# Optimization experiments

Hardware: AMD Instinct MI355X
Metric: run time of the kernel (lower is better)

The kernel has to match this reference:

```python
import jax, jax.numpy as jnp
import numpy as np

DET = 512       # detector bins
N_THETA = 180   # projection angles, theta = 0..179 degrees (1 deg spacing)


def _ramp_filter(size):
    """skimage _get_fourier_filter(size, 'ramp'): spatial ramp -> FFT."""
    n = np.concatenate((np.arange(1, size // 2 + 1, 2),
                        np.arange(size // 2 - 1, 0, -2)))
    f = np.zeros(size)
    f[0] = 0.25
    f[1::2] = -1.0 / (np.pi * n) ** 2
    return jnp.asarray(2.0 * np.real(np.fft.fft(f)), dtype=jnp.float32)


def _iradon(x):
    B, C, det, A = x.shape
    theta = jnp.deg2rad(jnp.arange(A, dtype=jnp.float32))  # 0..179 deg

    # --- ramp filtering along the detector axis ---
    size = max(64, int(2 ** np.ceil(np.log2(2 * det))))  # 1024 for det=512
    filt = _ramp_filter(size)                            # (size,)
    xp = jnp.pad(x, ((0, 0), (0, 0), (0, size - det), (0, 0)))
    proj_f = jnp.fft.fft(xp, axis=2) * filt[None, None, :, None]
    filtered = jnp.real(jnp.fft.ifft(proj_f, axis=2))[:, :, :det, :]  # (B,C,det,A)

    # --- backprojection (circle=False) ---
    out_size = int(np.floor(np.sqrt(det ** 2 / 2.0)))  # 362
    radius = out_size // 2
    xpr = jnp.arange(out_size, dtype=jnp.float32)[:, None] - radius  # rows
    ypr = jnp.arange(out_size, dtype=jnp.float32)[None, :] - radius  # cols
    cos_t = jnp.cos(theta)
    sin_t = jnp.sin(theta)
    # detector coordinate for every (angle, pixel): t = y*cos - x*sin
    t = ypr[None] * cos_t[:, None, None] - xpr[None] * sin_t[:, None, None]  # (A,out,out)
    pos = t + det // 2          # index into detector axis (x = arange(det)-det//2)
    i0 = jnp.floor(pos).astype(jnp.int32)
    frac = pos - i0.astype(jnp.float32)
    in_range = ((pos >= 0) & (pos <= det - 1)).astype(jnp.float32)  # fill_value=0 outside
    i0c = jnp.clip(i0, 0, det - 1)
    i1c = jnp.clip(i0 + 1, 0, det - 1)

    P = out_size * out_size
    ft = jnp.moveaxis(filtered, 3, 2)                     # (B,C,A,det)
    idx0 = jnp.broadcast_to(i0c.reshape(A, P)[None, None], (B, C, A, P))
    idx1 = jnp.broadcast_to(i1c.reshape(A, P)[None, None], (B, C, A, P))
    g0 = jnp.take_along_axis(ft, idx0, axis=3)            # (B,C,A,P)
    g1 = jnp.take_along_axis(ft, idx1, axis=3)
    w = frac.reshape(A, P)[None, None]
    m = in_range.reshape(A, P)[None, None]
    val = ((1.0 - w) * g0 + w * g1) * m                   # bilinear-in-1D interp, 0 outside
    recon = val.sum(axis=2).reshape(B, C, out_size, out_size)
    return recon * (jnp.pi / (2.0 * A))


def setup_inputs() -> dict:
    key = jax.random.key(0)
    x = jax.random.normal(key, (4, 1, DET, N_THETA), dtype=jnp.float32)
    return {"x": x}


def reference(x):
    return _iradon(x)
```

## Files before the change

### kernel.cpp

```cpp
#include <hip/hip_runtime.h>
#include <math.h>

#define DET 512
#define NA  180
#define OUT 362
#define RAD 181
#define OUTSQ (OUT * OUT)
#define NB  4

#define NSPLIT 12
#define APB    15
#define CHUNK  5
#define LQ     514

constexpr double PI_D = 3.14159265358979323846;

constexpr double tsin(double x) {
    double x2 = x * x;
    return x * (1.0 + x2 * (-1.0/6 + x2 * (1.0/120 + x2 * (-1.0/5040 +
               x2 * (1.0/362880 + x2 * (-1.0/39916800))))));
}
constexpr double tcos(double x) {
    double x2 = x * x;
    return 1.0 + x2 * (-0.5 + x2 * (1.0/24 + x2 * (-1.0/720 +
               x2 * (1.0/40320 + x2 * (-1.0/3628800)))));
}

struct Trig { float c[NA]; float s[NA]; };
constexpr Trig make_trig() {
    Trig t{};
    constexpr double r = PI_D / 180.0;
    for (int k = 0; k < NA; ++k) {
        double c, s;
        if (k <= 45)       { c =  tcos(k * r);          s =  tsin(k * r); }
        else if (k <= 90)  { c =  tsin((90 - k) * r);   s =  tcos((90 - k) * r); }
        else if (k <= 135) { c = -tsin((k - 90) * r);   s =  tcos((k - 90) * r); }
        else               { c = -tcos((180 - k) * r);  s =  tsin((180 - k) * r); }
        t.c[k] = (float)c; t.s[k] = (float)s;
    }
    return t;
}
__device__ constexpr Trig TRIG = make_trig();

__host__ __device__ constexpr float rampw0(int m) {
    int a = m < 0 ? -m : m;
    if (a > 511 || (a & 1) == 0) return 0.0f;
    double md = (double)a;
    return (float)(-2.0 / (PI_D * PI_D * md * md));
}

template<int R>
__device__ __forceinline__ void tap(const float* __restrict__ p,
        float& a0, float& a1, float& a2, float& a3) {
    const float v = p[R];
    if constexpr (rampw0(R)      != 0.0f) a0 = fmaf(rampw0(R),      v, a0);
    if constexpr (rampw0(R - 32) != 0.0f) a1 = fmaf(rampw0(R - 32), v, a1);
    if constexpr (rampw0(R - 64) != 0.0f) a2 = fmaf(rampw0(R - 64), v, a2);
    if constexpr (rampw0(R - 96) != 0.0f) a3 = fmaf(rampw0(R - 96), v, a3);
}

template<int R, int REND>
__device__ __forceinline__ void sweep(const float* __restrict__ p,
        float& a0, float& a1, float& a2, float& a3) {
    if constexpr (R <= REND) {
        tap<R>(p, a0, a1, a2, a3);
        sweep<R + 2, REND>(p, a0, a1, a2, a3);
    }
}

__global__ __launch_bounds__(512) void ramp_filter_kernel(
        const float* __restrict__ x, float* __restrict__ ft) {
    const int a   = blockIdx.x;
    const int b   = blockIdx.y;
    const int tid = threadIdx.x;
    const int t   = tid & 127;
    const int qtr = tid >> 7;
    const int q = (t & 31) + 128 * (t >> 5);

    __shared__ float xs[3 * DET];
    __shared__ float red[3][4][128];

    xs[tid]        = 0.0f;
    xs[1024 + tid] = 0.0f;
    xs[512 + tid]  = x[(b * DET + tid) * NA + a];
    __syncthreads();

    const float* p = xs + 512 + q;
    float a0 = 0.0f, a1 = 0.0f, a2 = 0.0f, a3 = 0.0f;

    if (qtr == 0) {
        a0 = 0.5f * p[0];
        a1 = 0.5f * p[32];
        a2 = 0.5f * p[64];
        a3 = 0.5f * p[96];
        sweep<-511, -233>(p, a0, a1, a2, a3);
    } else if (qtr == 1) {
        sweep<-231, 47>(p, a0, a1, a2, a3);
    } else if (qtr == 2) {
        sweep<49, 327>(p, a0, a1, a2, a3);
    } else {
        sweep<329, 607>(p, a0, a1, a2, a3);
    }
    if (qtr != 0) {
        red[qtr - 1][0][t] = a0;
        red[qtr - 1][1][t] = a1;
        red[qtr - 1][2][t] = a2;
        red[qtr - 1][3][t] = a3;
    }
    __syncthreads();

    if (qtr == 0) {
        float* ob = ft + ((size_t)a * DET + q) * NB + b;
        ob[0 * 4 * NB / 4 * 0] = 0.0f;
        ob[0]        = a0 + red[0][0][t] + red[1][0][t] + red[2][0][t];
        ob[32 * NB]  = a1 + red[0][1][t] + red[1][1][t] + red[2][1][t];
        ob[64 * NB]  = a2 + red[0][2][t] + red[1][2][t] + red[2][2][t];
        ob[96 * NB]  = a3 + red[0][3][t] + red[1][3][t] + red[2][3][t];
    }
}

__device__ __forceinline__ void acc4(float4& acc,
        const float4* __restrict__ L, float pos) {
    float pf = floorf(pos);
    float fr = pos - pf;
    int   i0 = (int)pf;
    const float4* q = (pos > (float)(DET - 1)) ? (L + DET) : (L + i0);
    float4 g0 = q[0];
    float4 g1 = q[1];
    acc.x += fmaf(fr, g1.x - g0.x, g0.x);
    acc.y += fmaf(fr, g1.y - g0.y, g0.y);
    acc.z += fmaf(fr, g1.z - g0.z, g0.z);
    acc.w += fmaf(fr, g1.w - g0.w, g0.w);
}

__global__ __launch_bounds__(256) void backproject_kernel(
        const float4* __restrict__ ftq, float* __restrict__ out) {
    const int sp = blockIdx.z;
    const int r0 = blockIdx.y * 32;
    const int c0 = blockIdx.x * 32;
    const int tid = threadIdx.x;
    const int tx = tid & 15;
    const int ty = tid >> 4;

    __shared__ float4 lines[CHUNK][LQ];

    if (tid < 2 * CHUNK)
        lines[tid >> 1][DET + (tid & 1)] = float4{0.0f, 0.0f, 0.0f, 0.0f};

    const float xpr = (float)(min(r0 + ty, OUT - 1) - RAD);
    const float ypr = (float)(min(c0 + tx, OUT - 1) - RAD);

    float4 a00 = {0,0,0,0}, a01 = {0,0,0,0}, a10 = {0,0,0,0}, a11 = {0,0,0,0};

    for (int rd = 0; rd < APB / CHUNK; ++rd) {
        __syncthreads();
        const float4* g = ftq + (size_t)(sp * APB + rd * CHUNK) * DET;
        #pragma unroll
        for (int k = 0; k < CHUNK * DET / 256; ++k) {
            int j = tid + k * 256;
            lines[j >> 9][j & 511] = g[j];
        }
        __syncthreads();

        const int abase = sp * APB + rd * CHUNK;
        #pragma unroll
        for (int i = 0; i < CHUNK; ++i) {
            const float cv = TRIG.c[abase + i];
            const float sv = TRIG.s[abase + i];
            float p00 = fmaf(ypr, cv, fmaf(xpr, -sv, 256.0f));
            float p01 = fmaf(16.0f, cv, p00);
            float p10 = fmaf(-16.0f, sv, p00);
            float p11 = fmaf(-16.0f, sv, p01);
            const float4* L = &lines[i][0];
            acc4(a00, L, p00);
            acc4(a01, L, p01);
            acc4(a10, L, p10);
            acc4(a11, L, p11);
        }
    }

    const float scale = (float)(PI_D / (2.0 * NA));
    const int r = r0 + ty;
    const int c = c0 + tx;

#define EMIT(ACC, RR, CC)                                          \
    if ((RR) < OUT && (CC) < OUT) {                                \
        const int off = (RR) * OUT + (CC);                         \
        atomicAdd(out + off,             (ACC).x * scale);         \
        atomicAdd(out + OUTSQ + off,     (ACC).y * scale);         \
        atomicAdd(out + 2 * OUTSQ + off, (ACC).z * scale);         \
        atomicAdd(out + 3 * OUTSQ + off, (ACC).w * scale);         \
    }
    EMIT(a00, r, c);
    EMIT(a01, r, c + 16);
    EMIT(a10, r + 16, c);
    EMIT(a11, r + 16, c + 16);
#undef EMIT
}

extern "C" void kernel_launch(void* const* d_in, const int* in_sizes, int n_in,
                              void* d_out, int out_size, void* d_ws, size_t ws_size,
                              hipStream_t stream) {
    const float* x = (const float*)d_in[0];
    float* ft  = (float*)d_ws;
    float* out = (float*)d_out;

    const int B = in_sizes[0] / (DET * NA);

    hipMemsetAsync(out, 0, (size_t)out_size * sizeof(float), stream);
    ramp_filter_kernel<<<dim3(NA, B), 512, 0, stream>>>(x, ft);
    backproject_kernel<<<dim3((OUT + 31) / 32, (OUT + 31) / 32, NSPLIT),
                         256, 0, stream>>>((const float4*)ft, out);
}
```

Measured before the change: 107.6 us.

## Restructure ramp filter to 8 outputs per thread and widen backprojection tiles

The ramp filter now splits the convolution across 8 tap ranges, with each thread computing 8 outputs spaced 64 bins apart, and reduces the partial sums through a larger shared array. This is meant to balance work per thread and cut redundant shared loads. Backprojection moves to 512-thread blocks covering 32x64 pixel tiles, with each thread handling 4 pixels in a row and a smaller angle chunk in shared memory. Fewer blocks reload the filtered lines, at the cost of higher register pressure, less parallelism in the reduction thread, and more wasted threads at the column edge.

```diff
diff --git a/kernel.cpp b/kernel.cpp
--- a/kernel.cpp
+++ b/kernel.cpp
@@ -10,7 +10,7 @@
 
 #define NSPLIT 12
 #define APB    15
-#define CHUNK  5
+#define CHUNK  3
 #define LQ     514
 
 constexpr double PI_D = 3.14159265358979323846;
@@ -50,21 +50,23 @@
 }
 
 template<int R>
-__device__ __forceinline__ void tap(const float* __restrict__ p,
-        float& a0, float& a1, float& a2, float& a3) {
+__device__ __forceinline__ void tap8(const float* __restrict__ p, float* acc) {
     const float v = p[R];
-    if constexpr (rampw0(R)      != 0.0f) a0 = fmaf(rampw0(R),      v, a0);
-    if constexpr (rampw0(R - 32) != 0.0f) a1 = fmaf(rampw0(R - 32), v, a1);
-    if constexpr (rampw0(R - 64) != 0.0f) a2 = fmaf(rampw0(R - 64), v, a2);
-    if constexpr (rampw0(R - 96) != 0.0f) a3 = fmaf(rampw0(R - 96), v, a3);
+    if constexpr (rampw0(R)       != 0.0f) acc[0] = fmaf(rampw0(R),       v, acc[0]);
+    if constexpr (rampw0(R - 64)  != 0.0f) acc[1] = fmaf(rampw0(R - 64),  v, acc[1]);
+    if constexpr (rampw0(R - 128) != 0.0f) acc[2] = fmaf(rampw0(R - 128), v, acc[2]);
+    if constexpr (rampw0(R - 192) != 0.0f) acc[3] = fmaf(rampw0(R - 192), v, acc[3]);
+    if constexpr (rampw0(R - 256) != 0.0f) acc[4] = fmaf(rampw0(R - 256), v, acc[4]);
+    if constexpr (rampw0(R - 320) != 0.0f) acc[5] = fmaf(rampw0(R - 320), v, acc[5]);
+    if constexpr (rampw0(R - 384) != 0.0f) acc[6] = fmaf(rampw0(R - 384), v, acc[6]);
+    if constexpr (rampw0(R - 448) != 0.0f) acc[7] = fmaf(rampw0(R - 448), v, acc[7]);
 }
 
 template<int R, int REND>
-__device__ __forceinline__ void sweep(const float* __restrict__ p,
-        float& a0, float& a1, float& a2, float& a3) {
+__device__ __forceinline__ void sweep8(const float* __restrict__ p, float* acc) {
     if constexpr (R <= REND) {
-        tap<R>(p, a0, a1, a2, a3);
-        sweep<R + 2, REND>(p, a0, a1, a2, a3);
+        tap8<R>(p, acc);
+        sweep8<R + 2, REND>(p, acc);
     }
 }
 
@@ -73,49 +75,47 @@
     const int a   = blockIdx.x;
     const int b   = blockIdx.y;
     const int tid = threadIdx.x;
-    const int t   = tid & 127;
-    const int qtr = tid >> 7;
-    const int q = (t & 31) + 128 * (t >> 5);
+    const int t   = tid & 63;
+    const int e   = tid >> 6;
 
     __shared__ float xs[3 * DET];
-    __shared__ float red[3][4][128];
+    __shared__ float red[7][8][64];
 
     xs[tid]        = 0.0f;
     xs[1024 + tid] = 0.0f;
     xs[512 + tid]  = x[(b * DET + tid) * NA + a];
     __syncthreads();
 
-    const float* p = xs + 512 + q;
-    float a0 = 0.0f, a1 = 0.0f, a2 = 0.0f, a3 = 0.0f;
-
-    if (qtr == 0) {
-        a0 = 0.5f * p[0];
-        a1 = 0.5f * p[32];
-        a2 = 0.5f * p[64];
-        a3 = 0.5f * p[96];
-        sweep<-511, -233>(p, a0, a1, a2, a3);
-    } else if (qtr == 1) {
-        sweep<-231, 47>(p, a0, a1, a2, a3);
-    } else if (qtr == 2) {
-        sweep<49, 327>(p, a0, a1, a2, a3);
-    } else {
-        sweep<329, 607>(p, a0, a1, a2, a3);
-    }
-    if (qtr != 0) {
-        red[qtr - 1][0][t] = a0;
-        red[qtr - 1][1][t] = a1;
-        red[qtr - 1][2][t] = a2;
-        red[qtr - 1][3][t] = a3;
+    const float* p = xs + 512 + t;
+    float acc[8] = {0.0f, 0.0f, 0.0f, 0.0f, 0.0f, 0.0f, 0.0f, 0.0f};
+
+    if (e == 0) {
+        #pragma unroll
+        for (int j = 0; j < 8; ++j) acc[j] = 0.5f * p[64 * j];
+        sweep8<-511, -329>(p, acc);
+    } else if (e == 1) { sweep8<-327, -145>(p, acc);
+    } else if (e == 2) { sweep8<-143,   39>(p, acc);
+    } else if (e == 3) { sweep8<  41,  223>(p, acc);
+    } else if (e == 4) { sweep8< 225,  407>(p, acc);
+    } else if (e == 5) { sweep8< 409,  591>(p, acc);
+    } else if (e == 6) { sweep8< 593,  775>(p, acc);
+    } else             { sweep8< 777,  959>(p, acc); }
+
+    if (e != 0) {
+        #pragma unroll
+        for (int j = 0; j < 8; ++j) red[e - 1][j][t] = acc[j];
     }
     __syncthreads();
 
-    if (qtr == 0) {
-        float* ob = ft + ((size_t)a * DET + q) * NB + b;
-        ob[0 * 4 * NB / 4 * 0] = 0.0f;
-        ob[0]        = a0 + red[0][0][t] + red[1][0][t] + red[2][0][t];
-        ob[32 * NB]  = a1 + red[0][1][t] + red[1][1][t] + red[2][1][t];
-        ob[64 * NB]  = a2 + red[0][2][t] + red[1][2][t] + red[2][2][t];
-        ob[96 * NB]  = a3 + red[0][3][t] + red[1][3][t] + red[2][3][t];
+    if (e == 0) {
+        float* ob = ft + ((size_t)a * DET + t) * NB + b;
+        #pragma unroll
+        for (int j = 0; j < 8; ++j) {
+            float s = acc[j];
+            #pragma unroll
+            for (int q7 = 0; q7 < 7; ++q7) s += red[q7][j][t];
+            ob[(size_t)(64 * j) * NB] = s;
+        }
     }
 }
 
@@ -133,11 +133,11 @@
     acc.w += fmaf(fr, g1.w - g0.w, g0.w);
 }
 
-__global__ __launch_bounds__(256) void backproject_kernel(
+__global__ __launch_bounds__(512, 6) void backproject_kernel(
         const float4* __restrict__ ftq, float* __restrict__ out) {
     const int sp = blockIdx.z;
     const int r0 = blockIdx.y * 32;
-    const int c0 = blockIdx.x * 32;
+    const int c0 = blockIdx.x * 64;
     const int tid = threadIdx.x;
     const int tx = tid & 15;
     const int ty = tid >> 4;
@@ -148,16 +148,16 @@
         lines[tid >> 1][DET + (tid & 1)] = float4{0.0f, 0.0f, 0.0f, 0.0f};
 
     const float xpr = (float)(min(r0 + ty, OUT - 1) - RAD);
-    const float ypr = (float)(min(c0 + tx, OUT - 1) - RAD);
-
-    float4 a00 = {0,0,0,0}, a01 = {0,0,0,0}, a10 = {0,0,0,0}, a11 = {0,0,0,0};
+    const float ypr = (float)(c0 + tx - RAD);
+
+    float4 A0 = {0,0,0,0}, A1 = {0,0,0,0}, A2 = {0,0,0,0}, A3 = {0,0,0,0};
 
     for (int rd = 0; rd < APB / CHUNK; ++rd) {
         __syncthreads();
         const float4* g = ftq + (size_t)(sp * APB + rd * CHUNK) * DET;
         #pragma unroll
-        for (int k = 0; k < CHUNK * DET / 256; ++k) {
-            int j = tid + k * 256;
+        for (int k = 0; k < CHUNK; ++k) {
+            int j = tid + k * 512;
             lines[j >> 9][j & 511] = g[j];
         }
         __syncthreads();
@@ -167,34 +167,33 @@
         for (int i = 0; i < CHUNK; ++i) {
             const float cv = TRIG.c[abase + i];
             const float sv = TRIG.s[abase + i];
-            float p00 = fmaf(ypr, cv, fmaf(xpr, -sv, 256.0f));
-            float p01 = fmaf(16.0f, cv, p00);
-            float p10 = fmaf(-16.0f, sv, p00);
-            float p11 = fmaf(-16.0f, sv, p01);
+            float p0 = fmaf(ypr, cv, fmaf(xpr, -sv, 256.0f));
+            float p1 = fmaf(16.0f, cv, p0);
+            float p2 = fmaf(32.0f, cv, p0);
+            float p3 = fmaf(48.0f, cv, p0);
             const float4* L = &lines[i][0];
-            acc4(a00, L, p00);
-            acc4(a01, L, p01);
-            acc4(a10, L, p10);
-            acc4(a11, L, p11);
+            acc4(A0, L, p0);
+            acc4(A1, L, p1);
+            acc4(A2, L, p2);
+            acc4(A3, L, p3);
         }
     }
 
     const float scale = (float)(PI_D / (2.0 * NA));
     const int r = r0 + ty;
-    const int c = c0 + tx;
-
-#define EMIT(ACC, RR, CC)                                          \
-    if ((RR) < OUT && (CC) < OUT) {                                \
-        const int off = (RR) * OUT + (CC);                         \
+
+#define EMIT(ACC, CC)                                              \
+    if (r < OUT && (CC) < OUT) {                                   \
+        const int off = r * OUT + (CC);                            \
         atomicAdd(out + off,             (ACC).x * scale);         \
         atomicAdd(out + OUTSQ + off,     (ACC).y * scale);         \
         atomicAdd(out + 2 * OUTSQ + off, (ACC).z * scale);         \
         atomicAdd(out + 3 * OUTSQ + off, (ACC).w * scale);         \
     }
-    EMIT(a00, r, c);
-    EMIT(a01, r, c + 16);
-    EMIT(a10, r + 16, c);
-    EMIT(a11, r + 16, c + 16);
+    EMIT(A0, c0 + tx);
+    EMIT(A1, c0 + tx + 16);
+    EMIT(A2, c0 + tx + 32);
+    EMIT(A3, c0 + tx + 48);
 #undef EMIT
 }
 
@@ -209,6 +208,6 @@
 
     hipMemsetAsync(out, 0, (size_t)out_size * sizeof(float), stream);
     ramp_filter_kernel<<<dim3(NA, B), 512, 0, stream>>>(x, ft);
-    backproject_kernel<<<dim3((OUT + 31) / 32, (OUT + 31) / 32, NSPLIT),
-                         256, 0, stream>>>((const float4*)ft, out);
-}
+    backproject_kernel<<<dim3((OUT + 63) / 64, (OUT + 31) / 32, NSPLIT),
+                         512, 0, stream>>>((const float4*)ft, out);
+}
```

New measurement: 118.6 us. 1.1x slower.

## Pad shared-memory line stride to 5 floats and halve ramp filter block

Applied to the files above, without the earlier changes.

The backprojection kernel now stores each detector bin's four batch values at a stride of five floats in shared memory instead of as packed float4s. This is meant to reduce LDS bank conflicts on the data-dependent gathers, at the cost of scalar loads instead of 128-bit loads. To fit the padded layout, the chunk of staged angles per round drops from five to three. The ramp filter kernel moves from 512 to 256 threads, with each thread doing twice as many taps and a smaller two-way reduction.

```diff
diff --git a/kernel.cpp b/kernel.cpp
--- a/kernel.cpp
+++ b/kernel.cpp
@@ -10,8 +10,9 @@
 
 #define NSPLIT 12
 #define APB    15
-#define CHUNK  5
-#define LQ     514
+#define CHUNK  3
+#define LSTR   5
+#define LLEN   (514 * LSTR)
 
 constexpr double PI_D = 3.14159265358979323846;
 
@@ -68,69 +69,66 @@
     }
 }
 
-__global__ __launch_bounds__(512) void ramp_filter_kernel(
+__global__ __launch_bounds__(256) void ramp_filter_kernel(
         const float* __restrict__ x, float* __restrict__ ft) {
     const int a   = blockIdx.x;
     const int b   = blockIdx.y;
     const int tid = threadIdx.x;
-    const int t   = tid & 127;
-    const int qtr = tid >> 7;
+    const int t    = tid & 127;
+    const int half = tid >> 7;
     const int q = (t & 31) + 128 * (t >> 5);
 
     __shared__ float xs[3 * DET];
-    __shared__ float red[3][4][128];
+    __shared__ float red[4 * 128];
 
     xs[tid]        = 0.0f;
+    xs[256 + tid]  = 0.0f;
     xs[1024 + tid] = 0.0f;
+    xs[1280 + tid] = 0.0f;
     xs[512 + tid]  = x[(b * DET + tid) * NA + a];
+    xs[768 + tid]  = x[(b * DET + 256 + tid) * NA + a];
     __syncthreads();
 
     const float* p = xs + 512 + q;
     float a0 = 0.0f, a1 = 0.0f, a2 = 0.0f, a3 = 0.0f;
 
-    if (qtr == 0) {
+    if (half == 0) {
         a0 = 0.5f * p[0];
         a1 = 0.5f * p[32];
         a2 = 0.5f * p[64];
         a3 = 0.5f * p[96];
-        sweep<-511, -233>(p, a0, a1, a2, a3);
-    } else if (qtr == 1) {
-        sweep<-231, 47>(p, a0, a1, a2, a3);
-    } else if (qtr == 2) {
-        sweep<49, 327>(p, a0, a1, a2, a3);
+        sweep<-511, 47>(p, a0, a1, a2, a3);
     } else {
-        sweep<329, 607>(p, a0, a1, a2, a3);
-    }
-    if (qtr != 0) {
-        red[qtr - 1][0][t] = a0;
-        red[qtr - 1][1][t] = a1;
-        red[qtr - 1][2][t] = a2;
-        red[qtr - 1][3][t] = a3;
+        sweep<49, 607>(p, a0, a1, a2, a3);
+        red[      t] = a0;
+        red[128 + t] = a1;
+        red[256 + t] = a2;
+        red[384 + t] = a3;
     }
     __syncthreads();
 
-    if (qtr == 0) {
+    if (half == 0) {
         float* ob = ft + ((size_t)a * DET + q) * NB + b;
-        ob[0 * 4 * NB / 4 * 0] = 0.0f;
-        ob[0]        = a0 + red[0][0][t] + red[1][0][t] + red[2][0][t];
-        ob[32 * NB]  = a1 + red[0][1][t] + red[1][1][t] + red[2][1][t];
-        ob[64 * NB]  = a2 + red[0][2][t] + red[1][2][t] + red[2][2][t];
-        ob[96 * NB]  = a3 + red[0][3][t] + red[1][3][t] + red[2][3][t];
+        ob[0]           = a0 + red[      t];
+        ob[32 * NB]     = a1 + red[128 + t];
+        ob[64 * NB]     = a2 + red[256 + t];
+        ob[96 * NB]     = a3 + red[384 + t];
     }
 }
 
 __device__ __forceinline__ void acc4(float4& acc,
-        const float4* __restrict__ L, float pos) {
+        const float* __restrict__ L, float pos) {
     float pf = floorf(pos);
     float fr = pos - pf;
     int   i0 = (int)pf;
-    const float4* q = (pos > (float)(DET - 1)) ? (L + DET) : (L + i0);
-    float4 g0 = q[0];
-    float4 g1 = q[1];
-    acc.x += fmaf(fr, g1.x - g0.x, g0.x);
-    acc.y += fmaf(fr, g1.y - g0.y, g0.y);
-    acc.z += fmaf(fr, g1.z - g0.z, g0.z);
-    acc.w += fmaf(fr, g1.w - g0.w, g0.w);
+    int   di = (pos > (float)(DET - 1)) ? (DET * LSTR) : (i0 * LSTR);
+    const float* qp = L + di;
+    float g0x = qp[0],        g0y = qp[1],        g0z = qp[2],        g0w = qp[3];
+    float g1x = qp[LSTR + 0], g1y = qp[LSTR + 1], g1z = qp[LSTR + 2], g1w = qp[LSTR + 3];
+    acc.x += fmaf(fr, g1x - g0x, g0x);
+    acc.y += fmaf(fr, g1y - g0y, g0y);
+    acc.z += fmaf(fr, g1z - g0z, g0z);
+    acc.w += fmaf(fr, g1w - g0w, g0w);
 }
 
 __global__ __launch_bounds__(256) void backproject_kernel(
@@ -142,15 +140,15 @@
     const int tx = tid & 15;
     const int ty = tid >> 4;
 
-    __shared__ float4 lines[CHUNK][LQ];
-
-    if (tid < 2 * CHUNK)
-        lines[tid >> 1][DET + (tid & 1)] = float4{0.0f, 0.0f, 0.0f, 0.0f};
+    __shared__ float lines[CHUNK][LLEN];
+
+    if (tid < CHUNK * 10)
+        lines[tid / 10][512 * LSTR + (tid % 10)] = 0.0f;
 
     const float xpr = (float)(min(r0 + ty, OUT - 1) - RAD);
     const float ypr = (float)(min(c0 + tx, OUT - 1) - RAD);
 
-    float4 a00 = {0,0,0,0}, a01 = {0,0,0,0}, a10 = {0,0,0,0}, a11 = {0,0,0,0};
+    float4 A00 = {0,0,0,0}, A01 = {0,0,0,0}, A10 = {0,0,0,0}, A11 = {0,0,0,0};
 
     for (int rd = 0; rd < APB / CHUNK; ++rd) {
         __syncthreads();
@@ -158,7 +156,9 @@
         #pragma unroll
         for (int k = 0; k < CHUNK * DET / 256; ++k) {
             int j = tid + k * 256;
-            lines[j >> 9][j & 511] = g[j];
+            float4 v = g[j];
+            float* w = &lines[j >> 9][(j & 511) * LSTR];
+            w[0] = v.x; w[1] = v.y; w[2] = v.z; w[3] = v.w;
         }
         __syncthreads();
 
@@ -171,11 +171,11 @@
             float p01 = fmaf(16.0f, cv, p00);
             float p10 = fmaf(-16.0f, sv, p00);
             float p11 = fmaf(-16.0f, sv, p01);
-            const float4* L = &lines[i][0];
-            acc4(a00, L, p00);
-            acc4(a01, L, p01);
-            acc4(a10, L, p10);
-            acc4(a11, L, p11);
+            const float* L = &lines[i][0];
+            acc4(A00, L, p00);
+            acc4(A01, L, p01);
+            acc4(A10, L, p10);
+            acc4(A11, L, p11);
         }
     }
 
@@ -191,10 +191,10 @@
         atomicAdd(out + 2 * OUTSQ + off, (ACC).z * scale);         \
         atomicAdd(out + 3 * OUTSQ + off, (ACC).w * scale);         \
     }
-    EMIT(a00, r, c);
-    EMIT(a01, r, c + 16);
-    EMIT(a10, r + 16, c);
-    EMIT(a11, r + 16, c + 16);
+    EMIT(A00, r, c);
+    EMIT(A01, r, c + 16);
+    EMIT(A10, r + 16, c);
+    EMIT(A11, r + 16, c + 16);
 #undef EMIT
 }
 
@@ -208,7 +208,7 @@
     const int B = in_sizes[0] / (DET * NA);
 
     hipMemsetAsync(out, 0, (size_t)out_size * sizeof(float), stream);
-    ramp_filter_kernel<<<dim3(NA, B), 512, 0, stream>>>(x, ft);
+    ramp_filter_kernel<<<dim3(NA, B), 256, 0, stream>>>(x, ft);
     backproject_kernel<<<dim3((OUT + 31) / 32, (OUT + 31) / 32, NSPLIT),
                          256, 0, stream>>>((const float4*)ft, out);
 }
```

Result: slower. 111.2 us (+3.3%).
